# Performance work log

Measured on AMD Instinct MI355X. Metric: run time of the kernel, lower is better.

## Reference

```python
import jax, jax.numpy as jnp
import numpy as np

KERNELS = (2, 3, 6, 7)
ALPHA = 2.0
DT = 1.0  # time=1.0, step_size=1.0 -> one RK4 (3/8 rule) step, as torchdiffeq 'rk4'


def _conv(x, w, b):
    # x: [B,C,N,L], w: [O,I,1,k] -> valid conv over time axis
    y = jax.lax.conv_general_dilated(x, w, (1, 1), 'VALID',
                                     dimension_numbers=('NCHW', 'OIHW', 'NCHW'))
    return y + b[None, :, None, None]


def _inception(x, ws, bs):
    outs = [_conv(x, w, b) for w, b in zip(ws, bs)]
    L = outs[-1].shape[-1]  # shortest output (largest kernel=7)
    return jnp.concatenate([o[..., -L:] for o in outs], axis=1)


def _norm_adj(adj):
    A = adj + jnp.eye(adj.shape[0], dtype=adj.dtype)
    dinv = A.sum(1) ** -0.5
    return dinv[:, None] * A * dinv[None, :]  # D^-1/2 (A+I) D^-1/2


def _cgp(x, A_norm, mw, mb):
    f = lambda y: 0.5 * ALPHA * (jnp.einsum('ncwl,vw->ncvl', y, A_norm) - y)
    k1 = f(x)
    y2 = x + (DT / 3.0) * k1
    k2 = f(y2)
    y3 = x + DT * (k2 - k1 / 3.0)
    k3 = f(y3)
    y4 = x + DT * (k1 - k2 + k3)
    k4 = f(y4)
    yf = x + (DT / 8.0) * (k1 + 3.0 * (k2 + k3) + k4)
    # odefunc.out collects the state at each of the 4 f-evals, plus final state
    cat = jnp.concatenate([x, y2, y3, y4, yf], axis=1)  # [B, 5C, N, L]
    return _conv(cat, mw, mb)


def setup_inputs() -> dict:
    key = jax.random.key(0)
    B, C, N, T = 8, 64, 512, 64
    cq = C // 4
    ks = jax.random.split(key, 24)
    d = {
        'x': jax.random.normal(ks[0], (B, C, N, T), dtype=jnp.float32),
        'adj': jax.random.uniform(ks[1], (N, N), dtype=jnp.float32),
    }
    i = 2
    for branch in ('i1', 'i2'):
        for j, k in enumerate(KERNELS):
            d[f'{branch}w{j}'] = 0.1 * jax.random.normal(ks[i], (cq, C, 1, k), dtype=jnp.float32); i += 1
            d[f'{branch}b{j}'] = 0.1 * jax.random.normal(ks[i], (cq,), dtype=jnp.float32); i += 1
    d['m1w'] = 0.1 * jax.random.normal(ks[i], (C, 5 * C, 1, 1), dtype=jnp.float32); i += 1
    d['m1b'] = 0.1 * jax.random.normal(ks[i], (C,), dtype=jnp.float32); i += 1
    d['m2w'] = 0.1 * jax.random.normal(ks[i], (C, 5 * C, 1, 1), dtype=jnp.float32); i += 1
    d['m2b'] = 0.1 * jax.random.normal(ks[i], (C,), dtype=jnp.float32)
    return d


def reference(x, adj,
              i1w0, i1b0, i1w1, i1b1, i1w2, i1b2, i1w3, i1b3,
              i2w0, i2b0, i2w1, i2b1, i2w2, i2b2, i2w3, i2b3,
              m1w, m1b, m2w, m2b):
    T = x.shape[-1]  # receptive_field
    filt = jnp.tanh(_inception(x, (i1w0, i1w1, i1w2, i1w3), (i1b0, i1b1, i1b2, i1b3)))
    gate = jax.nn.sigmoid(_inception(x, (i2w0, i2w1, i2w2, i2w3), (i2b0, i2b1, i2b2, i2b3)))
    h = filt * gate  # dropout is identity in eval mode
    An = _norm_adj(adj)
    AnT = _norm_adj(adj.T)
    h = _cgp(h, An, m1w, m1b) + _cgp(h, AnT, m2w, m2b)
    pad = T - h.shape[-1]
    return jnp.pad(h, ((0, 0), (0, 0), (0, 0), (pad, 0)))
```

## Files before the change

kernel.cpp:

```cpp
#include <hip/hip_runtime.h>
#include <math.h>

#define NN 512
#define BB 8
#define CC 64
#define TT 64
#define LL 58
#define CL (CC*LL)
#define BCL (BB*CC*LL)
#define SZ ((size_t)NN*BCL)

typedef _Float16 half8 __attribute__((ext_vector_type(8)));
typedef _Float16 half4 __attribute__((ext_vector_type(4)));
typedef float f32x4 __attribute__((ext_vector_type(4)));

__global__ __launch_bounds__(64) void prep_adj(const float* __restrict__ adj,
                                               float* __restrict__ dinv1,
                                               float* __restrict__ dinv2){
  int v = blockIdx.x;
  int lane = threadIdx.x;
  float rs = 0.f, cs = 0.f;
  for (int w = lane; w < NN; w += 64){
    rs += adj[v*NN + w];
    cs += adj[w*NN + v];
  }
  for (int off = 32; off > 0; off >>= 1){
    rs += __shfl_down(rs, off);
    cs += __shfl_down(cs, off);
  }
  if (lane == 0){
    dinv1[v] = 1.f / sqrtf(rs + 1.f);
    dinv2[v] = 1.f / sqrtf(cs + 1.f);
  }
}

__global__ __launch_bounds__(256) void build_norm(const float* __restrict__ adj,
                                                  const float* __restrict__ dinv1,
                                                  const float* __restrict__ dinv2,
                                                  _Float16* __restrict__ An,
                                                  _Float16* __restrict__ AnT){
  int v = blockIdx.x;
  float d1v = dinv1[v], d2v = dinv2[v];
  for (int w = threadIdx.x; w < NN; w += 256){
    float diag = (v == w) ? 1.f : 0.f;
    An[v*NN + w]  = (_Float16)(d1v * (adj[v*NN + w] + diag) * dinv1[w] - diag);
    AnT[v*NN + w] = (_Float16)(d2v * (adj[w*NN + v] + diag) * dinv2[w] - diag);
  }
}

__global__ __launch_bounds__(256) void u_prep(const float* __restrict__ W1,
                                              const float* __restrict__ W2,
                                              _Float16* __restrict__ U1,
                                              _Float16* __restrict__ U2){
  const float coef[5][5] = {
    {1.f, 1.f, 1.f, 1.f, 1.f},
    {0.f, 1.f/3.f, 2.f/3.f, 1.f, 1.f},
    {0.f, 0.f, 1.f/3.f, 1.f/3.f, 0.5f},
    {0.f, 0.f, 0.f, 1.f/3.f, 1.f/6.f},
    {0.f, 0.f, 0.f, 0.f, 1.f/24.f}};
  int idx = blockIdx.x*256 + threadIdx.x;
  int o = idx / 320, rem = idx - o*320;
  int d = rem >> 6, c = rem & 63;
  float a1 = 0.f, a2 = 0.f;
  #pragma unroll
  for (int s = 0; s < 5; ++s){
    float cf = coef[d][s];
    a1 += cf * W1[o*320 + s*64 + c];
    a2 += cf * W2[o*320 + s*64 + c];
  }
  U1[idx] = (_Float16)a1;
  U2[idx] = (_Float16)a2;
}

__global__ __launch_bounds__(448) void wfg_prep(
    const float* __restrict__ w10, const float* __restrict__ w11,
    const float* __restrict__ w12, const float* __restrict__ w13,
    const float* __restrict__ w20, const float* __restrict__ w21,
    const float* __restrict__ w22, const float* __restrict__ w23,
    const float* __restrict__ b10, const float* __restrict__ b11,
    const float* __restrict__ b12, const float* __restrict__ b13,
    const float* __restrict__ b20, const float* __restrict__ b21,
    const float* __restrict__ b22, const float* __restrict__ b23,
    _Float16* __restrict__ WfG, float* __restrict__ biasFG){
  int r = blockIdx.x;
  int t = threadIdx.x;
  int qp = t >> 6, ic = t & 63;
  int gate = r >> 6;
  int j = (r >> 4) & 3;
  int oc = r & 15;
  const int kjs[4] = {2, 3, 6, 7};
  int kj = kjs[j];
  const float* wsel = gate ? ((j==0)?w20:(j==1)?w21:(j==2)?w22:w23)
                           : ((j==0)?w10:(j==1)?w11:(j==2)?w12:w13);
  int off = 7 - kj;
  float val = (qp >= off) ? wsel[(oc*64 + ic)*kj + (qp - off)] : 0.f;
  WfG[(size_t)r*448 + t] = (_Float16)val;
  if (t == 0){
    const float* bsel = gate ? ((j==0)?b20:(j==1)?b21:(j==2)?b22:b23)
                             : ((j==0)?b10:(j==1)?b11:(j==2)?b12:b13);
    biasFG[r] = bsel[oc];
  }
}

__global__ __launch_bounds__(256) void xt_prep(const float* __restrict__ x,
                                               _Float16* __restrict__ xTg){
  __shared__ float T[64][65];
  int n = blockIdx.x;
  int b = blockIdx.y;
  int tid = threadIdx.x;
  #pragma unroll
  for (int r = 0; r < 4; ++r){
    int f = tid + r*256;
    int ic = f >> 4, t4 = f & 15;
    float4 v = *(const float4*)&x[(((size_t)(b*64 + ic))*512 + n)*64 + t4*4];
    T[ic][t4*4+0] = v.x; T[ic][t4*4+1] = v.y;
    T[ic][t4*4+2] = v.z; T[ic][t4*4+3] = v.w;
  }
  __syncthreads();
  #pragma unroll
  for (int r = 0; r < 2; ++r){
    int f = tid + r*256;
    int t = f >> 3, ch = f & 7;
    half8 hv;
    #pragma unroll
    for (int q2 = 0; q2 < 8; ++q2) hv[q2] = (_Float16)T[ch*8 + q2][t];
    *(half8*)&xTg[(((size_t)(b*64 + t))*512 + n)*64 + ch*8] = hv;
  }
}

__global__ __launch_bounds__(256, 2) void inception_mfma(
    const _Float16* __restrict__ xTg,
    const _Float16* __restrict__ WfG,
    const float* __restrict__ biasFG,
    _Float16* __restrict__ S_h){
  __shared__ _Float16 X[13*32*64];
  int nt = blockIdx.x;
  int lt = blockIdx.y;
  int b  = blockIdx.z;
  int n0 = nt*32, l0 = lt*7;
  int tid = threadIdx.x;

  int sch = tid & 7, sn = (tid >> 3) & 31;
  #pragma unroll
  for (int r = 0; r < 13; ++r){
    int t = l0 + r;
    half8 v = {};
    if (t < 64)
      v = *(const half8*)&xTg[(((size_t)(b*64 + t))*512 + n0 + sn)*64 + sch*8];
    *(half8*)&X[(size_t)(r*256 + sn*8 + (sch ^ (sn & 7)))*8] = v;
  }

  int w = tid >> 6, lane = tid & 63;
  int m = lane & 15, kg = lane >> 4;

  f32x4 aF0[7] = {}, aG0[7] = {}, aF1[7] = {}, aG1[7] = {};

  __syncthreads();

  const _Float16* wb = WfG + (size_t)(w*16 + m)*448 + kg*8;
  for (int ch = 0; ch < 2; ++ch){
    half8 wF7[7], wG7[7];
    #pragma unroll
    for (int d = 0; d < 7; ++d){
      wF7[d] = *(const half8*)(wb + (2*d + ch)*32);
      wG7[d] = *(const half8*)(wb + (size_t)64*448 + (2*d + ch)*32);
    }
    int c0 = ch*4 + kg;
    int xoff = m*64 + (c0 ^ (m & 7))*8;
    #pragma unroll
    for (int td = 0; td < 13; ++td){
      half8 b0 = *(const half8*)&X[td*2048 + xoff];
      half8 b1 = *(const half8*)&X[td*2048 + 1024 + xoff];
      #pragma unroll
      for (int d = 0; d < 7; ++d){
        if (d <= td && d >= td - 6){
          int ll = td - d;
          aF0[ll] = __builtin_amdgcn_mfma_f32_16x16x32_f16(wF7[d], b0, aF0[ll], 0, 0, 0);
          aG0[ll] = __builtin_amdgcn_mfma_f32_16x16x32_f16(wG7[d], b0, aG0[ll], 0, 0, 0);
          aF1[ll] = __builtin_amdgcn_mfma_f32_16x16x32_f16(wF7[d], b1, aF1[ll], 0, 0, 0);
          aG1[ll] = __builtin_amdgcn_mfma_f32_16x16x32_f16(wG7[d], b1, aG1[ll], 0, 0, 0);
        }
      }
    }
  }

  f32x4 bF = *(const f32x4*)&biasFG[w*16 + kg*4];
  f32x4 bG = *(const f32x4*)&biasFG[64 + w*16 + kg*4];

  #pragma unroll
  for (int ll = 0; ll < 7; ++ll){
    int l = l0 + ll;
    if (l < LL){
      #pragma unroll
      for (int rr = 0; rr < 4; ++rr){
        int c = w*16 + kg*4 + rr;
        float F0 = aF0[ll][rr] + bF[rr];
        float G0 = aG0[ll][rr] + bG[rr];
        float F1 = aF1[ll][rr] + bF[rr];
        float G1 = aG1[ll][rr] + bG[rr];
        float h0 = (2.f*__builtin_amdgcn_rcpf(1.f + __expf(-2.f*F0)) - 1.f)
                 * __builtin_amdgcn_rcpf(1.f + __expf(-G0));
        float h1 = (2.f*__builtin_amdgcn_rcpf(1.f + __expf(-2.f*F1)) - 1.f)
                 * __builtin_amdgcn_rcpf(1.f + __expf(-G1));
        size_t base = ((size_t)(b*64 + c)*LL + l)*NN + n0;
        S_h[base + m]      = (_Float16)h0;
        S_h[base + 16 + m] = (_Float16)h1;
      }
    }
  }
}

__device__ __forceinline__ void gll16(const _Float16* g, _Float16* l){
  __builtin_amdgcn_global_load_lds(
      (const __attribute__((address_space(1))) unsigned int*)g,
      (__attribute__((address_space(3))) unsigned int*)l, 16, 0, 0);
}
#define BAR() asm volatile("s_barrier" ::: "memory")

__global__ __launch_bounds__(256, 2) void gemm_z2(
    int nx,
    const _Float16* __restrict__ A0, const _Float16* __restrict__ B0,
    _Float16* __restrict__ O0,
    const _Float16* __restrict__ A1, const _Float16* __restrict__ B1,
    _Float16* __restrict__ O1){
  __shared__ _Float16 L[32768];

  int bid = blockIdx.x;
  int q8 = gridDim.x >> 3;
  int virt = (bid & 7)*q8 + (bid >> 3);
  int y = virt & 1;
  int pair = virt >> 1;
  int x = pair % nx;
  int z = pair / nx;

  const _Float16* __restrict__ A = z ? A1 : A0;
  const _Float16* __restrict__ B = z ? B1 : B0;
  _Float16* __restrict__ O = z ? O1 : O0;

  const int m0 = x * 128;
  const int v0 = y * 256;
  const int tid = threadIdx.x;
  const int ww = tid >> 6;
  const int lane = tid & 63;
  const int lr = lane & 15;
  const int kg = lane >> 4;
  const int wvq = ww & 1;
  const int wmq = ww >> 1;

  const int srow = lane >> 2;
  const int gch  = ((lane & 3) - ((lane >> 3) & 3)) & 3;
  const _Float16* gAb = A + (size_t)(v0 + ww*64 + srow)*NN + gch*8;
  const _Float16* gBb = B + (size_t)(m0 + ww*32 + srow)*NN + gch*8;

  #define STAGE(buf, kt)                                                    \
    { char* lA_ = (char*)L + (buf)*24576 + ww*4096;                         \
      char* lB_ = (char*)L + (buf)*24576 + 16384 + ww*2048;                 \
      const _Float16* gA_ = gAb + (kt)*32;                                  \
      const _Float16* gB_ = gBb + (kt)*32;                                  \
      _Pragma("unroll")                                                     \
      for (int s_ = 0; s_ < 4; ++s_)                                        \
        gll16(gA_ + (size_t)s_*16*NN, (_Float16*)(lA_ + s_*1024));          \
      _Pragma("unroll")                                                     \
      for (int s_ = 0; s_ < 2; ++s_)                                        \
        gll16(gB_ + (size_t)s_*16*NN, (_Float16*)(lB_ + s_*1024)); }

  const int slot = (kg + (lr >> 1)) & 3;
  const int aOff = (wvq*128 + lr)*64 + slot*16;
  const int bOff = 16384 + (wmq*64 + lr)*64 + slot*16;

  half8 af[8], bf[4];
  f32x4 acc[8][4] = {};

  STAGE(0, 0)
  STAGE(1, 1)
  asm volatile("s_waitcnt vmcnt(6)" ::: "memory");
  BAR();

  #pragma unroll
  for (int kt = 0; kt < 16; ++kt){
    const int buf = kt & 1;
    char* lb = (char*)L + buf*24576;
    #pragma unroll
    for (int i = 0; i < 8; ++i) af[i] = *(const half8*)(lb + aOff + i*1024);
    #pragma unroll
    for (int j = 0; j < 4; ++j) bf[j] = *(const half8*)(lb + bOff + j*1024);
    asm volatile("s_waitcnt lgkmcnt(0)" ::: "memory");
    BAR();
    if (kt + 2 < 16) STAGE(buf, kt + 2)

    __builtin_amdgcn_s_setprio(1);
    #pragma unroll
    for (int i = 0; i < 8; ++i)
      #pragma unroll
      for (int j = 0; j < 4; ++j)
        acc[i][j] = __builtin_amdgcn_mfma_f32_16x16x32_f16(af[i], bf[j], acc[i][j], 0, 0, 0);
    __builtin_amdgcn_s_setprio(0);

    if (kt < 14){
      asm volatile("s_waitcnt vmcnt(6)" ::: "memory");
      BAR();
    } else if (kt == 14){
      asm volatile("s_waitcnt vmcnt(0)" ::: "memory");
      BAR();
    }
  }
  #undef STAGE

  char* Lw = (char*)L + ww*16384;
  #pragma unroll
  for (int j = 0; j < 4; ++j){
    int row = j*16 + lr;
    #pragma unroll
    for (int i = 0; i < 8; ++i){
      int c = (i*4 + kg) ^ ((lr & 7)*4);
      half4 oq;
      #pragma unroll
      for (int rr = 0; rr < 4; ++rr) oq[rr] = (_Float16)acc[i][j][rr];
      *(half4*)(Lw + row*256 + c*8) = oq;
    }
  }
  #pragma unroll
  for (int s = 0; s < 16; ++s){
    int row = s*4 + kg;
    int cc = (2*lr) ^ ((row & 7)*4);
    half8 hv = *(const half8*)(Lw + row*256 + cc*8);
    *(half8*)&O[(size_t)(m0 + wmq*64 + row)*NN + v0 + wvq*128 + lr*8] = hv;
  }
}

template<int PASS>
__global__ __launch_bounds__(256, 3) void combine_mfma(
    const _Float16* __restrict__ Sh, const _Float16* __restrict__ S2,
    const _Float16* __restrict__ S3, const _Float16* __restrict__ S4,
    const _Float16* __restrict__ Sf,
    const _Float16* __restrict__ Wc,
    const float* __restrict__ bias,
    _Float16* __restrict__ tmp){
  __shared__ __align__(16) _Float16 Xt[256*64];
  __shared__ float Bsh[64];
  int v0 = blockIdx.x * 256;
  int l  = blockIdx.y;
  int b  = blockIdx.z;
  int tid = threadIdx.x;
  int w = tid >> 6, lane = tid & 63;
  int lr = lane & 15, kg = lane >> 4;

  if (tid < 64) Bsh[tid] = bias[tid];

  const int c0  = ((tid >> 3) & 7) * 8;
  const int lv0 = (tid & 7) * 8 + w * 64;
  const int wslot = (c0 >> 3) ^ (((lv0 >> 3) & 1) << 2);
  const int rx = ((lr >> 3) & 1) << 2;

  const _Float16* Sarr[5] = {Sh, S2, S3, S4, Sf};
  f32x4 acc[4][4] = {};

  for (int kt = 0; kt < 5; ++kt){
    const _Float16* S = Sarr[kt];
    unsigned xr[8][4];
    const _Float16* gbase = &S[((size_t)(b*64 + c0)*58 + l)*512 + v0 + lv0];
    #pragma unroll
    for (int r = 0; r < 8; ++r)
      *(uint4*)xr[r] = *(const uint4*)(gbase + (size_t)r*58*512);

    __syncthreads();

    #pragma unroll
    for (int q = 0; q < 8; ++q){
      const unsigned sel = (q & 1) ? 0x07060302u : 0x05040100u;
      const int d2 = q >> 1;
      uint4 y;
      y.x = __builtin_amdgcn_perm(xr[1][d2], xr[0][d2], sel);
      y.y = __builtin_amdgcn_perm(xr[3][d2], xr[2][d2], sel);
      y.z = __builtin_amdgcn_perm(xr[5][d2], xr[4][d2], sel);
      y.w = __builtin_amdgcn_perm(xr[7][d2], xr[6][d2], sel);
      *(uint4*)((char*)Xt + (lv0 + q)*128 + wslot*16) = y;
    }

    half8 aW[2][4];
    #pragma unroll
    for (int ks = 0; ks < 2; ++ks)
      #pragma unroll
      for (int jj = 0; jj < 4; ++jj)
        aW[ks][jj] = *(const half8*)&Wc[(size_t)(jj*16 + lr)*320
                                        + kt*64 + ks*32 + kg*8];

    __syncthreads();

    #pragma unroll
    for (int ks = 0; ks < 2; ++ks){
      #pragma unroll
      for (int vt = 0; vt < 4; ++vt){
        half8 bf = *(const half8*)((char*)Xt + (w*64 + vt*16 + lr)*128
                                   + ((ks*4 + kg) ^ rx)*16);
        #pragma unroll
        for (int jj = 0; jj < 4; ++jj)
          acc[vt][jj] = __builtin_amdgcn_mfma_f32_16x16x32_f16(
              aW[ks][jj], bf, acc[vt][jj], 0, 0, 0);
      }
    }
  }

  size_t rowbase = ((size_t)b*58 + l)*64;
  #pragma unroll
  for (int jj = 0; jj < 4; ++jj){
    #pragma unroll
    for (int rr = 0; rr < 4; ++rr){
      int o = jj*16 + kg*4 + rr;
      float bv = Bsh[o];
      size_t obase = (rowbase + o)*512 + v0 + w*64 + lr;
      #pragma unroll
      for (int vt = 0; vt < 4; ++vt){
        float val = acc[vt][jj][rr] + bv;
        size_t addr = obase + vt*16;
        if (PASS == 0) tmp[addr] = (_Float16)val;
        else           tmp[addr] = (_Float16)((float)tmp[addr] + val);
      }
    }
  }
}

__global__ __launch_bounds__(256) void untranspose(const _Float16* __restrict__ tmp,
                                                   float* __restrict__ out){
  __shared__ float T[58][65];
  int o = blockIdx.x;
  int b = blockIdx.y;
  int v0 = blockIdx.z * 64;
  int t = threadIdx.x;
  for (int idx = t; idx < 58*64; idx += 256){
    int lr = idx >> 6, vv = idx & 63;
    T[lr][vv] = (float)tmp[((size_t)(b*58 + lr)*64 + o)*NN + v0 + vv];
  }
  __syncthreads();
  #pragma unroll
  for (int i = 0; i < 16; ++i){
    int c = t + i*256;
    int vv = c >> 6, tt = c & 63;
    float val = (tt < 6) ? 0.f : T[tt - 6][vv];
    out[((size_t)(b*64 + o)*NN + v0 + vv)*TT + tt] = val;
  }
}

extern "C" void kernel_launch(void* const* d_in, const int* in_sizes, int n_in,
                              void* d_out, int out_size, void* d_ws, size_t ws_size,
                              hipStream_t stream){
  const float* x   = (const float*)d_in[0];
  const float* adj = (const float*)d_in[1];
  const float* w1[4] = {(const float*)d_in[2],  (const float*)d_in[4],
                        (const float*)d_in[6],  (const float*)d_in[8]};
  const float* b1[4] = {(const float*)d_in[3],  (const float*)d_in[5],
                        (const float*)d_in[7],  (const float*)d_in[9]};
  const float* w2[4] = {(const float*)d_in[10], (const float*)d_in[12],
                        (const float*)d_in[14], (const float*)d_in[16]};
  const float* b2[4] = {(const float*)d_in[11], (const float*)d_in[13],
                        (const float*)d_in[15], (const float*)d_in[17]};
  const float* m1w = (const float*)d_in[18];
  const float* m1b = (const float*)d_in[19];
  const float* m2w = (const float*)d_in[20];
  const float* m2b = (const float*)d_in[21];

  char* wsb = (char*)d_ws;
  float* dinv1 = (float*)(wsb);
  float* dinv2 = (float*)(wsb + 2048);
  _Float16* U1  = (_Float16*)(wsb + 4096);
  _Float16* U2  = (_Float16*)(wsb + 4096 + 40960);
  _Float16* Mn  = (_Float16*)(wsb + 167936);
  _Float16* MnT = (_Float16*)(wsb + 167936 + 524288);
  size_t sbytes = SZ * 2;
  char* sbase = wsb + 1216512;
  _Float16* S_h = (_Float16*)(sbase);
  _Float16* S2  = (_Float16*)(sbase + sbytes);
  _Float16* S3  = (_Float16*)(sbase + 2*sbytes);
  _Float16* S4  = (_Float16*)(sbase + 3*sbytes);
  _Float16* S5  = (_Float16*)(sbase + 4*sbytes);
  _Float16* tmp = (_Float16*)(sbase + 5*sbytes);
  _Float16* xTg = S2;
  _Float16* WfG = (_Float16*)(sbase + 6*sbytes);
  float* biasFG = (float*)(sbase + 6*sbytes + 114688);
  _Float16* M2  = (_Float16*)(sbase + 6*sbytes + 131072);
  _Float16* MT2 = (_Float16*)(sbase + 6*sbytes + 131072 + 524288);
  float* out = (float*)d_out;

  prep_adj<<<NN, 64, 0, stream>>>(adj, dinv1, dinv2);
  build_norm<<<NN, 256, 0, stream>>>(adj, dinv1, dinv2, Mn, MnT);
  gemm_z2<<<16, 256, 0, stream>>>(4, MnT, Mn, M2, Mn, MnT, MT2);
  u_prep<<<80, 256, 0, stream>>>(m1w, m2w, U1, U2);
  wfg_prep<<<128, 448, 0, stream>>>(
      w1[0],w1[1],w1[2],w1[3], w2[0],w2[1],w2[2],w2[3],
      b1[0],b1[1],b1[2],b1[3], b2[0],b2[1],b2[2],b2[3], WfG, biasFG);
  xt_prep<<<dim3(NN, BB), 256, 0, stream>>>(x, xTg);
  inception_mfma<<<dim3(16, 9, 8), 256, 0, stream>>>(xTg, WfG, biasFG, S_h);

  dim3 gc(2, LL, BB);
  for (int pass = 0; pass < 2; ++pass){
    const _Float16* Mp  = pass ? MnT : Mn;
    const _Float16* Mp2 = pass ? MT2 : M2;
    gemm_z2<<<928, 256, 0, stream>>>(232, Mp, S_h, S2, Mp2, S_h, S3);
    gemm_z2<<<928, 256, 0, stream>>>(232, Mp2, S2, S4, Mp2, S3, S5);
    if (pass == 0)
      combine_mfma<0><<<gc, 256, 0, stream>>>(S_h, S2, S3, S4, S5, U1, m1b, tmp);
    else
      combine_mfma<1><<<gc, 256, 0, stream>>>(S_h, S2, S3, S4, S5, U2, m2b, tmp);
  }
  untranspose<<<dim3(64, 8, 8), 256, 0, stream>>>(tmp, out);
}
```

Baseline: 473.5 us.

## Halve inception node tile and restructure MFMA loop for occupancy

The inception kernel now handles 16 nodes per block instead of 32, which halves the shared-memory tile and the accumulator registers, doubles the grid, and raises launch bounds to 3 blocks per CU. The inner loop is reorganised to iterate over weight slices and output positions, reloading B fragments from LDS for each MFMA rather than reusing them across two node halves. The aim is more occupancy and more blocks to fill the GPU, at the cost of extra LDS reads and weight fragment loads per output.

```diff
diff --git a/kernel.cpp b/kernel.cpp
--- a/kernel.cpp
+++ b/kernel.cpp
@@ -128,58 +128,60 @@
   }
 }
 
-__global__ __launch_bounds__(256, 2) void inception_mfma(
+__global__ __launch_bounds__(256, 3) void inception_mfma(
     const _Float16* __restrict__ xTg,
     const _Float16* __restrict__ WfG,
     const float* __restrict__ biasFG,
     _Float16* __restrict__ S_h){
-  __shared__ _Float16 X[13*32*64];
+  __shared__ _Float16 X[13*16*64];
   int nt = blockIdx.x;
   int lt = blockIdx.y;
   int b  = blockIdx.z;
-  int n0 = nt*32, l0 = lt*7;
+  int n0 = nt*16, l0 = lt*7;
   int tid = threadIdx.x;
 
-  int sch = tid & 7, sn = (tid >> 3) & 31;
-  #pragma unroll
-  for (int r = 0; r < 13; ++r){
-    int t = l0 + r;
-    half8 v = {};
-    if (t < 64)
-      v = *(const half8*)&xTg[(((size_t)(b*64 + t))*512 + n0 + sn)*64 + sch*8];
-    *(half8*)&X[(size_t)(r*256 + sn*8 + (sch ^ (sn & 7)))*8] = v;
+  int inner = tid & 127;
+  int sr = tid >> 7;
+  int sch = inner & 7, sn = (inner >> 3) & 15;
+  #pragma unroll
+  for (int r = 0; r < 7; ++r){
+    int row = r*2 + sr;
+    if (row < 13){
+      int t = l0 + row;
+      half8 v = {};
+      if (t < 64)
+        v = *(const half8*)&xTg[(((size_t)(b*64 + t))*512 + n0 + sn)*64 + sch*8];
+      *(half8*)&X[(size_t)(row*128 + sn*8 + (sch ^ (sn & 7)))*8] = v;
+    }
   }
 
   int w = tid >> 6, lane = tid & 63;
   int m = lane & 15, kg = lane >> 4;
 
-  f32x4 aF0[7] = {}, aG0[7] = {}, aF1[7] = {}, aG1[7] = {};
+  f32x4 aF[7] = {}, aG[7] = {};
 
   __syncthreads();
 
   const _Float16* wb = WfG + (size_t)(w*16 + m)*448 + kg*8;
-  for (int ch = 0; ch < 2; ++ch){
+  #pragma unroll
+  for (int sh = 0; sh < 2; ++sh){
     half8 wF7[7], wG7[7];
     #pragma unroll
     for (int d = 0; d < 7; ++d){
-      wF7[d] = *(const half8*)(wb + (2*d + ch)*32);
-      wG7[d] = *(const half8*)(wb + (size_t)64*448 + (2*d + ch)*32);
-    }
-    int c0 = ch*4 + kg;
-    int xoff = m*64 + (c0 ^ (m & 7))*8;
-    #pragma unroll
-    for (int td = 0; td < 13; ++td){
-      half8 b0 = *(const half8*)&X[td*2048 + xoff];
-      half8 b1 = *(const half8*)&X[td*2048 + 1024 + xoff];
-      #pragma unroll
-      for (int d = 0; d < 7; ++d){
-        if (d <= td && d >= td - 6){
-          int ll = td - d;
-          aF0[ll] = __builtin_amdgcn_mfma_f32_16x16x32_f16(wF7[d], b0, aF0[ll], 0, 0, 0);
-          aG0[ll] = __builtin_amdgcn_mfma_f32_16x16x32_f16(wG7[d], b0, aG0[ll], 0, 0, 0);
-          aF1[ll] = __builtin_amdgcn_mfma_f32_16x16x32_f16(wF7[d], b1, aF1[ll], 0, 0, 0);
-          aG1[ll] = __builtin_amdgcn_mfma_f32_16x16x32_f16(wG7[d], b1, aG1[ll], 0, 0, 0);
-        }
+      wF7[d] = *(const half8*)(wb + (sh*7 + d)*32);
+      wG7[d] = *(const half8*)(wb + (size_t)64*448 + (sh*7 + d)*32);
+    }
+    #pragma unroll
+    for (int d = 0; d < 7; ++d){
+      int s = sh*7 + d;
+      int tb = s >> 1;
+      int c0 = (s & 1)*4 + kg;
+      int xoff = m*8 + (c0 ^ (m & 7));
+      #pragma unroll
+      for (int ll = 0; ll < 7; ++ll){
+        half8 b0 = *(const half8*)&X[(size_t)((ll + tb)*128 + xoff)*8];
+        aF[ll] = __builtin_amdgcn_mfma_f32_16x16x32_f16(wF7[d], b0, aF[ll], 0, 0, 0);
+        aG[ll] = __builtin_amdgcn_mfma_f32_16x16x32_f16(wG7[d], b0, aG[ll], 0, 0, 0);
       }
     }
   }
@@ -194,17 +196,12 @@
       #pragma unroll
       for (int rr = 0; rr < 4; ++rr){
         int c = w*16 + kg*4 + rr;
-        float F0 = aF0[ll][rr] + bF[rr];
-        float G0 = aG0[ll][rr] + bG[rr];
-        float F1 = aF1[ll][rr] + bF[rr];
-        float G1 = aG1[ll][rr] + bG[rr];
+        float F0 = aF[ll][rr] + bF[rr];
+        float G0 = aG[ll][rr] + bG[rr];
         float h0 = (2.f*__builtin_amdgcn_rcpf(1.f + __expf(-2.f*F0)) - 1.f)
                  * __builtin_amdgcn_rcpf(1.f + __expf(-G0));
-        float h1 = (2.f*__builtin_amdgcn_rcpf(1.f + __expf(-2.f*F1)) - 1.f)
-                 * __builtin_amdgcn_rcpf(1.f + __expf(-G1));
         size_t base = ((size_t)(b*64 + c)*LL + l)*NN + n0;
-        S_h[base + m]      = (_Float16)h0;
-        S_h[base + 16 + m] = (_Float16)h1;
+        S_h[base + m] = (_Float16)h0;
       }
     }
   }
@@ -489,7 +486,7 @@
       w1[0],w1[1],w1[2],w1[3], w2[0],w2[1],w2[2],w2[3],
       b1[0],b1[1],b1[2],b1[3], b2[0],b2[1],b2[2],b2[3], WfG, biasFG);
   xt_prep<<<dim3(NN, BB), 256, 0, stream>>>(x, xTg);
-  inception_mfma<<<dim3(16, 9, 8), 256, 0, stream>>>(xTg, WfG, biasFG, S_h);
+  inception_mfma<<<dim3(32, 9, 8), 256, 0, stream>>>(xTg, WfG, biasFG, S_h);
 
   dim3 gc(2, LL, BB);
   for (int pass = 0; pass < 2; ++pass){
```

Result: no change. 466.3 us (-1.5%).
